# Kernel optimization log

Measured on AMD Instinct MI355X. Metric: run time of the kernel, lower is better.

Reference implementation:

```python
import jax, jax.numpy as jnp
import numpy as np

WS = 7       # window_size
SHIFT = 3    # shift_size
NH = 12      # num_heads
DIM = 384
EPS = 1e-5


def _rel_pos_index():
    coords = np.stack(np.meshgrid(np.arange(WS), np.arange(WS), indexing='ij'))  # [2,WS,WS]
    cf = coords.reshape(2, -1)
    rel = cf[:, :, None] - cf[:, None, :]              # [2,N,N]
    rel = rel.transpose(1, 2, 0)
    rel[:, :, 0] += WS - 1
    rel[:, :, 1] += WS - 1
    rel[:, :, 0] *= 2 * WS - 1
    return jnp.asarray(rel.sum(-1))                    # [N,N] int


def _attn_mask(H, W):
    img = np.zeros((H, W), dtype=np.float32)
    cnt = 0
    sl = (slice(0, -WS), slice(-WS, -SHIFT), slice(-SHIFT, None))
    for hs in sl:
        for ws in sl:
            img[hs, ws] = cnt
            cnt += 1
    mw = img.reshape(H // WS, WS, W // WS, WS).transpose(0, 2, 1, 3).reshape(-1, WS * WS)  # [nW,N]
    am = mw[:, None, :] - mw[:, :, None]
    am = np.where(am != 0, -100.0, 0.0).astype(np.float32)
    return jnp.asarray(am)                             # [nW,N,N]


def _ln(x, g, b):
    mu = jnp.mean(x, -1, keepdims=True)
    var = jnp.mean(jnp.square(x - mu), -1, keepdims=True)
    return (x - mu) * jax.lax.rsqrt(var + EPS) * g + b


def setup_inputs() -> dict:
    key = jax.random.key(0)
    ks = jax.random.split(key, 8)
    B, H, W, C = 32, 56, 56, DIM
    s = lambda fan: 1.0 / np.sqrt(fan)
    return {
        'x': jax.random.normal(ks[0], (B, H * W, C), jnp.float32),
        'ln1_g': jnp.ones((C,), jnp.float32), 'ln1_b': jnp.zeros((C,), jnp.float32),
        'qkv_w': jax.random.normal(ks[1], (C, 3 * C), jnp.float32) * s(C),
        'qkv_b': jnp.zeros((3 * C,), jnp.float32),
        'proj_w': jax.random.normal(ks[2], (C, C), jnp.float32) * s(C),
        'proj_b': jnp.zeros((C,), jnp.float32),
        'bias_table': jax.random.normal(ks[3], ((2 * WS - 1) ** 2, NH), jnp.float32) * 0.02,
        'ln2_g': jnp.ones((C,), jnp.float32), 'ln2_b': jnp.zeros((C,), jnp.float32),
        'fc1_w': jax.random.normal(ks[4], (C, 4 * C), jnp.float32) * s(C),
        'fc1_b': jnp.zeros((4 * C,), jnp.float32),
        'fc2_w': jax.random.normal(ks[5], (4 * C, C), jnp.float32) * s(4 * C),
        'fc2_b': jnp.zeros((C,), jnp.float32),
        'H': H, 'W': W,
    }


def reference(x, ln1_g, ln1_b, qkv_w, qkv_b, proj_w, proj_b, bias_table,
              ln2_g, ln2_b, fc1_w, fc1_b, fc2_w, fc2_b, H, W):
    B, L, C = x.shape
    N = WS * WS
    hd = C // NH
    scale = hd ** -0.5
    rel_idx = _rel_pos_index()
    mask = _attn_mask(H, W)          # [nW,N,N]
    nW = (H // WS) * (W // WS)

    shortcut = x
    h = _ln(x, ln1_g, ln1_b).reshape(B, H, W, C)
    h = jnp.roll(h, (-SHIFT, -SHIFT), axis=(1, 2))
    # window partition -> [B*nW, N, C]
    h = h.reshape(B, H // WS, WS, W // WS, WS, C).transpose(0, 1, 3, 2, 4, 5)
    h = h.reshape(B * nW, N, C)

    qkv = (h @ qkv_w + qkv_b).reshape(B * nW, N, 3, NH, hd).transpose(2, 0, 3, 1, 4)
    q, k, v = qkv[0] * scale, qkv[1], qkv[2]           # [B_,NH,N,hd]
    attn = jnp.einsum('bhnd,bhmd->bhnm', q, k)          # [B_,NH,N,N]
    rpb = bias_table[rel_idx].transpose(2, 0, 1)        # [NH,N,N]
    attn = attn + rpb[None]
    attn = attn.reshape(B, nW, NH, N, N) + mask[None, :, None]
    attn = jax.nn.softmax(attn.reshape(B * nW, NH, N, N), axis=-1)
    o = jnp.einsum('bhnm,bhmd->bhnd', attn, v).transpose(0, 2, 1, 3).reshape(B * nW, N, C)
    o = o @ proj_w + proj_b

    # window reverse + unshift
    o = o.reshape(B, H // WS, W // WS, WS, WS, C).transpose(0, 1, 3, 2, 4, 5).reshape(B, H, W, C)
    o = jnp.roll(o, (SHIFT, SHIFT), axis=(1, 2)).reshape(B, L, C)

    x = shortcut + o
    m = _ln(x, ln2_g, ln2_b)
    m = jax.nn.gelu(m @ fc1_w + fc1_b, approximate=False) @ fc2_w + fc2_b
    return x + m
```

## Files before the change

kernel.cpp:

```cpp
#include <hip/hip_runtime.h>
#include <hip/hip_bf16.h>
#include <math.h>

typedef __hip_bfloat16 bf16;
typedef __attribute__((ext_vector_type(8))) __bf16 bf16x8;
typedef __attribute__((ext_vector_type(4))) float f32x4;

#define SHIFT 3
#define TOK_TOTAL 100352
#define WIN_TOTAL 2048
#define BM_ELEMS (4 * 12 * 49 * 52)
#define PSTR 72

__device__ __forceinline__ bool is_f32(const void* flagp) {
  return ((const unsigned*)flagp)[0] == 0x3F800000u;
}
__device__ __forceinline__ float ldf(const void* p, size_t i, bool f32) {
  return f32 ? ((const float*)p)[i]
             : __bfloat162float(((const bf16*)p)[i]);
}

__global__ void cvt_small(const void* s0, const void* s1, const void* s2,
                          const void* s3, const void* s4, const void* s5,
                          const void* s6, const void* s7, const void* s8,
                          bf16* __restrict__ dst) {
  const bool f32 = is_f32(s0);
  int idx = blockIdx.x * 256 + threadIdx.x;
  if (idx >= 7020) return;
  const void* src; int off;
  if      (idx < 384)  { src = s0; off = 0; }
  else if (idx < 768)  { src = s1; off = 384; }
  else if (idx < 1920) { src = s2; off = 768; }
  else if (idx < 2304) { src = s3; off = 1920; }
  else if (idx < 4332) { src = s4; off = 2304; }
  else if (idx < 4716) { src = s5; off = 4332; }
  else if (idx < 5100) { src = s6; off = 4716; }
  else if (idx < 6636) { src = s7; off = 5100; }
  else                 { src = s8; off = 6636; }
  dst[idx] = __float2bfloat16(ldf(src, idx - off, f32));
}

__global__ void build_bm(const bf16* __restrict__ btab, bf16* __restrict__ bm) {
  int idx = blockIdx.x * 256 + threadIdx.x;
  if (idx >= 4 * 12 * 2401) return;
  int ch = idx / 2401, rem = idx - ch * 2401;
  int cls = ch / 12, head = ch - cls * 12;
  int q = rem / 49, k = rem - q * 49;
  int i1 = q / 7, j1 = q - 7 * i1;
  int i2 = k / 7, j2 = k - 7 * i2;
  int rel = (i1 - i2 + 6) * 13 + (j1 - j2 + 6);
  float v = __bfloat162float(btab[rel * 12 + head]);
  int rh1 = (cls & 2) ? (i1 < 4 ? 1 : 2) : 0;
  int rw1 = (cls & 1) ? (j1 < 4 ? 1 : 2) : 0;
  int rh2 = (cls & 2) ? (i2 < 4 ? 1 : 2) : 0;
  int rw2 = (cls & 1) ? (j2 < 4 ? 1 : 2) : 0;
  if (rh1 * 3 + rw1 != rh2 * 3 + rw2) v -= 100.0f;
  bm[(ch * 49 + q) * 52 + k] = __float2bfloat16(v);
}

__global__ void wt_transpose(const void* __restrict__ in, bf16* __restrict__ out,
                             int K, int N, const void* flagp) {
  const bool f32 = is_f32(flagp);
  int idx = blockIdx.x * 256 + threadIdx.x;
  if (idx < K * N) {
    int k = idx / N, n = idx - k * N;
    out[(size_t)n * K + k] = __float2bfloat16(ldf(in, idx, f32));
  }
}

__global__ __launch_bounds__(256) void ln1_impl(
    const void* __restrict__ x, const bf16* __restrict__ g,
    const bf16* __restrict__ b, bf16* __restrict__ h, int tokoff,
    const void* flagp) {
  const bool f32 = is_f32(flagp);
  int local = blockIdx.x * 4 + (threadIdx.x >> 6);
  int token = tokoff + local;
  int lane = threadIdx.x & 63;
  int w = token / 49, n = token - w * 49;
  int bb = w >> 6, iw = w & 63;
  int wh = iw >> 3, ww = iw & 7;
  int i = n / 7, j = n - i * 7;
  int sr = wh * 7 + i + SHIFT; if (sr >= 56) sr -= 56;
  int sc = ww * 7 + j + SHIFT; if (sc >= 56) sc -= 56;
  size_t base = ((size_t)bb * 3136 + (size_t)sr * 56 + sc) * 384;
  float v[6];
  float sum = 0.f, sq = 0.f;
#pragma unroll
  for (int t = 0; t < 6; t++) {
    v[t] = ldf(x, base + t * 64 + lane, f32);
    sum += v[t]; sq += v[t] * v[t];
  }
#pragma unroll
  for (int off = 32; off > 0; off >>= 1) {
    sum += __shfl_xor(sum, off);
    sq  += __shfl_xor(sq, off);
  }
  float mean = sum * (1.f / 384.f);
  float var  = sq * (1.f / 384.f) - mean * mean;
  float rstd = rsqrtf(var + 1e-5f);
  bf16* hp = h + (size_t)local * 384;
#pragma unroll
  for (int t = 0; t < 6; t++) {
    int c = t * 64 + lane;
    float y = (v[t] - mean) * rstd * __bfloat162float(g[c]) + __bfloat162float(b[c]);
    hp[c] = __float2bfloat16(y);
  }
}

__global__ __launch_bounds__(256) void ln2_kernel(
    const bf16* __restrict__ x1, const bf16* __restrict__ g,
    const bf16* __restrict__ b, bf16* __restrict__ out) {
  int local = blockIdx.x * 4 + (threadIdx.x >> 6);
  int lane = threadIdx.x & 63;
  const bf16* xp = x1 + (size_t)local * 384;
  float v[6];
  float sum = 0.f, sq = 0.f;
#pragma unroll
  for (int t = 0; t < 6; t++) {
    v[t] = __bfloat162float(xp[t * 64 + lane]);
    sum += v[t]; sq += v[t] * v[t];
  }
#pragma unroll
  for (int off = 32; off > 0; off >>= 1) {
    sum += __shfl_xor(sum, off);
    sq  += __shfl_xor(sq, off);
  }
  float mean = sum * (1.f / 384.f);
  float var  = sq * (1.f / 384.f) - mean * mean;
  float rstd = rsqrtf(var + 1e-5f);
  bf16* op = out + (size_t)local * 384;
#pragma unroll
  for (int t = 0; t < 6; t++) {
    int c = t * 64 + lane;
    float y = (v[t] - mean) * rstd * __bfloat162float(g[c]) + __bfloat162float(b[c]);
    op[c] = __float2bfloat16(y);
  }
}

template <int MODE>
__global__ __launch_bounds__(256, 2) void gemm128(
    const bf16* __restrict__ A, const bf16* __restrict__ Wt,
    const bf16* __restrict__ bias, void* __restrict__ outp,
    const void* __restrict__ extra, int K, int N, int tokoff,
    const void* flagp, int lbmask) {
  __shared__ bf16 As[128 * 40];
  __shared__ bf16 Bs[128 * 40];
  const int tid = threadIdx.x;
  const int wave = tid >> 6, lane = tid & 63;
  const int wm = (wave >> 1) * 64, wn = (wave & 1) * 64;
  const int lrow = lane & 15, lquad = lane >> 4;
  const int m0 = blockIdx.x * 128, n0 = blockIdx.y * 128;

  f32x4 acc[4][4] = {};

  const int arow = tid >> 2;
  const int acol = (tid & 3) * 8;
  const bf16* Ag = A + (size_t)(m0 + arow) * K + acol;
  const bf16* Bg = Wt + (size_t)(n0 + arow) * K + acol;
  const int ldso = arow * 40 + acol;

  for (int k0 = 0; k0 < K; k0 += 32) {
    float4 av0 = *(const float4*)(Ag + k0);
    float4 av1 = *(const float4*)(Ag + (size_t)64 * K + k0);
    float4 bv0 = *(const float4*)(Bg + k0);
    float4 bv1 = *(const float4*)(Bg + (size_t)64 * K + k0);
    __syncthreads();
    *(float4*)(As + ldso) = av0;
    *(float4*)(As + ldso + 64 * 40) = av1;
    *(float4*)(Bs + ldso) = bv0;
    *(float4*)(Bs + ldso + 64 * 40) = bv1;
    __syncthreads();
    bf16x8 af[4], bfr[4];
#pragma unroll
    for (int mi = 0; mi < 4; mi++)
      af[mi] = *(const bf16x8*)(As + (wm + mi * 16 + lrow) * 40 + lquad * 8);
#pragma unroll
    for (int ni = 0; ni < 4; ni++)
      bfr[ni] = *(const bf16x8*)(Bs + (wn + ni * 16 + lrow) * 40 + lquad * 8);
#pragma unroll
    for (int mi = 0; mi < 4; mi++)
#pragma unroll
      for (int ni = 0; ni < 4; ni++)
        acc[mi][ni] = __builtin_amdgcn_mfma_f32_16x16x32_bf16(
            af[mi], bfr[ni], acc[mi][ni], 0, 0, 0);
  }

  float bv[4];
#pragma unroll
  for (int ni = 0; ni < 4; ni++)
    bv[ni] = __bfloat162float(bias[n0 + wn + ni * 16 + lrow]);

  const bool f32 = (MODE == 1 || MODE == 3) ? is_f32(flagp) : false;

#pragma unroll
  for (int mi = 0; mi < 4; mi++) {
#pragma unroll
    for (int r = 0; r < 4; r++) {
      int row = m0 + wm + mi * 16 + lquad * 4 + r;
      if constexpr (MODE == 1) {
        bf16* xo = (bf16*)outp;
        int gtok = tokoff + row;
        int w = gtok / 49, n = gtok - w * 49;
        int bb = w >> 6, iw = w & 63;
        int wh = iw >> 3, ww = iw & 7;
        int i = n / 7, j = n - i * 7;
        int rr = wh * 7 + i + SHIFT; if (rr >= 56) rr -= 56;
        int cc = ww * 7 + j + SHIFT; if (cc >= 56) cc -= 56;
        int lb = bb & lbmask;
        size_t dloc = ((size_t)lb * 3136 + (size_t)rr * 56 + cc) * 384;
        size_t dglb = ((size_t)bb * 3136 + (size_t)rr * 56 + cc) * 384;
#pragma unroll
        for (int ni = 0; ni < 4; ni++) {
          int col = n0 + wn + ni * 16 + lrow;
          float v = acc[mi][ni][r] + bv[ni] + ldf(extra, dglb + col, f32);
          xo[dloc + col] = __float2bfloat16(v);
        }
      } else if constexpr (MODE == 3) {
        const bf16* x1 = (const bf16*)extra;
#pragma unroll
        for (int ni = 0; ni < 4; ni++) {
          int col = n0 + wn + ni * 16 + lrow;
          float v = acc[mi][ni][r] + bv[ni] + __bfloat162float(x1[(size_t)row * 384 + col]);
          size_t gi = (size_t)(tokoff + row) * 384 + col;
          if (f32) ((float*)outp)[gi] = v;
          else     ((bf16*)outp)[gi] = __float2bfloat16(v);
        }
      } else {
        bf16* xo = (bf16*)outp;
#pragma unroll
        for (int ni = 0; ni < 4; ni++) {
          int col = n0 + wn + ni * 16 + lrow;
          float v = acc[mi][ni][r] + bv[ni];
          if constexpr (MODE == 2)
            v = 0.5f * v * (1.0f + erff(v * 0.70710678118654752f));
          xo[(size_t)row * N + col] = __float2bfloat16(v);
        }
      }
    }
  }
}

__global__ __launch_bounds__(256) void attn_mfma(
    const bf16* __restrict__ qkv, const bf16* __restrict__ bm,
    bf16* __restrict__ out) {
  __shared__ bf16 pbuf[4][16 * PSTR];
  const int tid = threadIdx.x;
  const int wave = tid >> 6, lane = tid & 63;
  const int g = lane >> 4, lr = lane & 15;
  const int pair = blockIdx.x * 4 + wave;
  const int lw = pair / 12, head = pair - lw * 12;
  const int iw = lw & 63;
  const int wh = iw >> 3, ww = iw & 7;
  const int cls = ((wh == 7) ? 2 : 0) + ((ww == 7) ? 1 : 0);
  const bf16* bmh = bm + (size_t)(cls * 12 + head) * 49 * 52;
  const size_t qbase = (size_t)lw * 49 * 1152 + head * 32;
  bf16* pb = pbuf[wave];

  bf16x8 kf[4];
#pragma unroll
  for (int kj = 0; kj < 4; kj++) {
    int row = 16 * kj + lr; if (row > 48) row = 48;
    kf[kj] = *(const bf16x8*)(qkv + qbase + 384 + (size_t)row * 1152 + g * 8);
  }
  bf16x8 vf[2][2];
#pragma unroll
  for (int ks = 0; ks < 2; ks++)
#pragma unroll
    for (int di = 0; di < 2; di++) {
      union { bf16x8 v; short s[8]; } u;
#pragma unroll
      for (int j = 0; j < 8; j++) {
        int k = 32 * ks + 8 * g + j; if (k > 48) k = 48;
        u.s[j] = *(const short*)(qkv + qbase + 768 + (size_t)k * 1152 + 16 * di + lr);
      }
      vf[ks][di] = u.v;
    }

#pragma unroll
  for (int qi = 0; qi < 4; qi++) {
    int qrow = 16 * qi + lr; if (qrow > 48) qrow = 48;
    bf16x8 qf = *(const bf16x8*)(qkv + qbase + (size_t)qrow * 1152 + g * 8);
    f32x4 s[4] = {};
#pragma unroll
    for (int kj = 0; kj < 4; kj++)
      s[kj] = __builtin_amdgcn_mfma_f32_16x16x32_bf16(qf, kf[kj], s[kj], 0, 0, 0);

    float bmv[4][4];
#pragma unroll
    for (int r = 0; r < 4; r++) {
      int q = 16 * qi + 4 * g + r; if (q > 48) q = 48;
      const bf16* bmrow = bmh + q * 52;
#pragma unroll
      for (int kj = 0; kj < 4; kj++)
        bmv[r][kj] = __bfloat162float(bmrow[16 * kj + lr]);
    }

    float pexp[4][4];
    float inv[4];
#pragma unroll
    for (int r = 0; r < 4; r++) {
      float a[4];
#pragma unroll
      for (int kj = 0; kj < 4; kj++) {
        int k = 16 * kj + lr;
        a[kj] = (k < 49) ? fmaf(s[kj][r], 0.17677669529663687f, bmv[r][kj])
                         : -1e30f;
      }
      float m = fmaxf(fmaxf(a[0], a[1]), fmaxf(a[2], a[3]));
#pragma unroll
      for (int off = 8; off > 0; off >>= 1) m = fmaxf(m, __shfl_xor(m, off));
      float sum = 0.f;
#pragma unroll
      for (int kj = 0; kj < 4; kj++) {
        float e = __expf(a[kj] - m);
        pexp[kj][r] = e; sum += e;
      }
#pragma unroll
      for (int off = 8; off > 0; off >>= 1) sum += __shfl_xor(sum, off);
      inv[r] = 1.0f / sum;
    }

#pragma unroll
    for (int kj = 0; kj < 4; kj++)
#pragma unroll
      for (int r = 0; r < 4; r++)
        pb[(4 * g + r) * PSTR + 16 * kj + lr] = __float2bfloat16(pexp[kj][r]);

    bf16x8 pf0 = *(const bf16x8*)(pb + lr * PSTR + g * 8);
    bf16x8 pf1 = *(const bf16x8*)(pb + lr * PSTR + 32 + g * 8);

    f32x4 o[2] = {};
    o[0] = __builtin_amdgcn_mfma_f32_16x16x32_bf16(pf0, vf[0][0], o[0], 0, 0, 0);
    o[0] = __builtin_amdgcn_mfma_f32_16x16x32_bf16(pf1, vf[1][0], o[0], 0, 0, 0);
    o[1] = __builtin_amdgcn_mfma_f32_16x16x32_bf16(pf0, vf[0][1], o[1], 0, 0, 0);
    o[1] = __builtin_amdgcn_mfma_f32_16x16x32_bf16(pf1, vf[1][1], o[1], 0, 0, 0);

#pragma unroll
    for (int r = 0; r < 4; r++) {
      int q = 16 * qi + 4 * g + r;
      if (q < 49) {
#pragma unroll
        for (int di = 0; di < 2; di++)
          out[(size_t)(lw * 49 + q) * 384 + head * 32 + 16 * di + lr] =
              __float2bfloat16(o[di][r] * inv[r]);
      }
    }
  }
}

extern "C" void kernel_launch(void* const* d_in, const int* in_sizes, int n_in,
                              void* d_out, int out_size, void* d_ws, size_t ws_size,
                              hipStream_t stream) {
  const void* x          = d_in[0];
  const void* ln1_g      = d_in[1];
  const void* ln1_b      = d_in[2];
  const void* qkv_w      = d_in[3];
  const void* qkv_b      = d_in[4];
  const void* proj_w     = d_in[5];
  const void* proj_b     = d_in[6];
  const void* bias_table = d_in[7];
  const void* ln2_g      = d_in[8];
  const void* ln2_b      = d_in[9];
  const void* fc1_w      = d_in[10];
  const void* fc1_b      = d_in[11];
  const void* fc2_w      = d_in[12];
  const void* fc2_b      = d_in[13];

  char* ws = (char*)d_ws;
  bf16* qkv_wt  = (bf16*)ws;
  bf16* proj_wt = qkv_wt + 1152 * 384;
  bf16* fc1_wt  = proj_wt + 384 * 384;
  bf16* fc2_wt  = fc1_wt + 1536 * 384;
  bf16* small   = fc2_wt + 384 * 1536;
  bf16* bmtab   = small + 8192;
  char* p = (char*)(bmtab + BM_ELEMS + 64);

  const size_t fixedB = (size_t)(p - ws);
  int nchunk = 16;
  for (int n = 1; n <= 16; n <<= 1) {
    size_t need = fixedB + (size_t)(TOK_TOTAL / n) * 4608;
    if (need <= ws_size) { nchunk = n; break; }
  }
  const int CH   = TOK_TOTAL / nchunk;
  const int CWIN = WIN_TOTAL / nchunk;
  const int lbmask = 32 / nchunk - 1;

  bf16* buf1   = (bf16*)p;
  bf16* buf_x1 = (bf16*)(p + (size_t)CH * 384 * 2);
  bf16* buf2   = (bf16*)(p + (size_t)CH * 384 * 4);

  const bf16* c_ln1g = small;
  const bf16* c_ln1b = small + 384;
  const bf16* c_qkvb = small + 768;
  const bf16* c_projb = small + 1920;
  const bf16* c_btab = small + 2304;
  const bf16* c_ln2g = small + 4332;
  const bf16* c_ln2b = small + 4716;
  const bf16* c_fc1b = small + 5100;
  const bf16* c_fc2b = small + 6636;

  cvt_small<<<dim3(28), 256, 0, stream>>>(ln1_g, ln1_b, qkv_b, proj_b, bias_table,
                                          ln2_g, ln2_b, fc1_b, fc2_b, small);
  build_bm<<<dim3((4 * 12 * 2401 + 255) / 256), 256, 0, stream>>>(c_btab, bmtab);

  wt_transpose<<<dim3((384 * 1152 + 255) / 256), 256, 0, stream>>>(qkv_w, qkv_wt, 384, 1152, ln1_g);
  wt_transpose<<<dim3((384 * 384  + 255) / 256), 256, 0, stream>>>(proj_w, proj_wt, 384, 384, ln1_g);
  wt_transpose<<<dim3((384 * 1536 + 255) / 256), 256, 0, stream>>>(fc1_w, fc1_wt, 384, 1536, ln1_g);
  wt_transpose<<<dim3((1536 * 384 + 255) / 256), 256, 0, stream>>>(fc2_w, fc2_wt, 1536, 384, ln1_g);

  for (int c = 0; c < nchunk; c++) {
    const int tokoff = c * CH;

    ln1_impl<<<dim3(CH / 4), 256, 0, stream>>>(x, c_ln1g, c_ln1b, buf1, tokoff, ln1_g);

    gemm128<0><<<dim3(CH / 128, 9), 256, 0, stream>>>(
        buf1, qkv_wt, c_qkvb, buf2, nullptr, 384, 1152, 0, ln1_g, 0);

    attn_mfma<<<dim3(CWIN * 12 / 4), 256, 0, stream>>>(buf2, bmtab, buf1);

    gemm128<1><<<dim3(CH / 128, 3), 256, 0, stream>>>(
        buf1, proj_wt, c_projb, buf_x1, x, 384, 384, tokoff, ln1_g, lbmask);

    ln2_kernel<<<dim3(CH / 4), 256, 0, stream>>>(buf_x1, c_ln2g, c_ln2b, buf1);

    gemm128<2><<<dim3(CH / 128, 12), 256, 0, stream>>>(
        buf1, fc1_wt, c_fc1b, buf2, nullptr, 384, 1536, 0, ln1_g, 0);

    gemm128<3><<<dim3(CH / 128, 3), 256, 0, stream>>>(
        buf2, fc2_wt, c_fc2b, d_out, buf_x1, 1536, 384, tokoff, ln1_g, 0);
  }
}
```

Before: 1.258 ms.

## Fuse MLP fc1+GELU+fc2 into one kernel and swap GEMM grid axes

Replaces the separate fc1 (with GELU) and fc2 GEMM launches with one fused kernel. Each block handles 64 tokens, computes 128-wide slices of the hidden activation into LDS, applies GELU, and accumulates the fc2 product directly. This removes the large hidden-activation round trip through global memory and cuts the workspace need, which may allow fewer chunks. Separately, the remaining GEMMs now use the N tiles as the fast grid axis so neighbouring blocks share A rows. The cost is that fc2 weights are read straight from global memory with no LDS staging, and the 64-token tile gives less reuse per block.

```diff
diff --git a/kernel.cpp b/kernel.cpp
--- a/kernel.cpp
+++ b/kernel.cpp
@@ -149,7 +149,7 @@
   const int wave = tid >> 6, lane = tid & 63;
   const int wm = (wave >> 1) * 64, wn = (wave & 1) * 64;
   const int lrow = lane & 15, lquad = lane >> 4;
-  const int m0 = blockIdx.x * 128, n0 = blockIdx.y * 128;
+  const int m0 = blockIdx.y * 128, n0 = blockIdx.x * 128;
 
   f32x4 acc[4][4] = {};
 
@@ -190,7 +190,7 @@
   for (int ni = 0; ni < 4; ni++)
     bv[ni] = __bfloat162float(bias[n0 + wn + ni * 16 + lrow]);
 
-  const bool f32 = (MODE == 1 || MODE == 3) ? is_f32(flagp) : false;
+  const bool f32 = (MODE == 1) ? is_f32(flagp) : false;
 
 #pragma unroll
   for (int mi = 0; mi < 4; mi++) {
@@ -215,29 +215,122 @@
           float v = acc[mi][ni][r] + bv[ni] + ldf(extra, dglb + col, f32);
           xo[dloc + col] = __float2bfloat16(v);
         }
-      } else if constexpr (MODE == 3) {
-        const bf16* x1 = (const bf16*)extra;
-#pragma unroll
-        for (int ni = 0; ni < 4; ni++) {
-          int col = n0 + wn + ni * 16 + lrow;
-          float v = acc[mi][ni][r] + bv[ni] + __bfloat162float(x1[(size_t)row * 384 + col]);
-          size_t gi = (size_t)(tokoff + row) * 384 + col;
-          if (f32) ((float*)outp)[gi] = v;
-          else     ((bf16*)outp)[gi] = __float2bfloat16(v);
-        }
       } else {
         bf16* xo = (bf16*)outp;
 #pragma unroll
         for (int ni = 0; ni < 4; ni++) {
           int col = n0 + wn + ni * 16 + lrow;
           float v = acc[mi][ni][r] + bv[ni];
-          if constexpr (MODE == 2)
-            v = 0.5f * v * (1.0f + erff(v * 0.70710678118654752f));
           xo[(size_t)row * N + col] = __float2bfloat16(v);
         }
       }
     }
   }
+}
+
+__global__ __launch_bounds__(256, 2) void mlp_fused(
+    const bf16* __restrict__ A,
+    const bf16* __restrict__ W1t,
+    const bf16* __restrict__ W2t,
+    const bf16* __restrict__ b1,
+    const bf16* __restrict__ b2,
+    const bf16* __restrict__ x1,
+    void* __restrict__ outp, int tokoff, const void* flagp) {
+  __shared__ bf16 As[64 * 40];
+  __shared__ bf16 Bs[128 * 40];
+  __shared__ bf16 Pl[64 * 136];
+  const int tid = threadIdx.x;
+  const int wave = tid >> 6, lane = tid & 63;
+  const int lr = lane & 15, g = lane >> 4;
+  const int tok0 = blockIdx.x * 64;
+
+  f32x4 acc2[4][6] = {};
+
+  const int srow = tid >> 2, scol = (tid & 3) * 8;
+  const bf16* Ag = A + (size_t)(tok0 + srow) * 384 + scol;
+  const int ldso = srow * 40 + scol;
+
+  for (int kk = 0; kk < 12; kk++) {
+    f32x4 pacc[4][2] = {};
+    const bf16* Bg = W1t + (size_t)(kk * 128 + srow) * 384 + scol;
+    for (int k0 = 0; k0 < 384; k0 += 32) {
+      float4 av  = *(const float4*)(Ag + k0);
+      float4 bv0 = *(const float4*)(Bg + k0);
+      float4 bv1 = *(const float4*)(Bg + (size_t)64 * 384 + k0);
+      __syncthreads();
+      *(float4*)(As + ldso) = av;
+      *(float4*)(Bs + ldso) = bv0;
+      *(float4*)(Bs + ldso + 64 * 40) = bv1;
+      __syncthreads();
+      bf16x8 af[4], bw[2];
+#pragma unroll
+      for (int mi = 0; mi < 4; mi++)
+        af[mi] = *(const bf16x8*)(As + (mi * 16 + lr) * 40 + g * 8);
+#pragma unroll
+      for (int ni = 0; ni < 2; ni++)
+        bw[ni] = *(const bf16x8*)(Bs + (wave * 32 + ni * 16 + lr) * 40 + g * 8);
+#pragma unroll
+      for (int mi = 0; mi < 4; mi++)
+#pragma unroll
+        for (int ni = 0; ni < 2; ni++)
+          pacc[mi][ni] = __builtin_amdgcn_mfma_f32_16x16x32_bf16(
+              af[mi], bw[ni], pacc[mi][ni], 0, 0, 0);
+    }
+    float b1v[2];
+#pragma unroll
+    for (int ni = 0; ni < 2; ni++)
+      b1v[ni] = __bfloat162float(b1[kk * 128 + wave * 32 + ni * 16 + lr]);
+#pragma unroll
+    for (int mi = 0; mi < 4; mi++)
+#pragma unroll
+      for (int ni = 0; ni < 2; ni++)
+#pragma unroll
+        for (int r = 0; r < 4; r++) {
+          float v = pacc[mi][ni][r] + b1v[ni];
+          v = 0.5f * v * (1.0f + erff(v * 0.70710678118654752f));
+          Pl[(mi * 16 + g * 4 + r) * 136 + wave * 32 + ni * 16 + lr] =
+              __float2bfloat16(v);
+        }
+    __syncthreads();
+    const int kb = kk * 128;
+#pragma unroll
+    for (int kk2 = 0; kk2 < 4; kk2++) {
+      bf16x8 pf[4];
+#pragma unroll
+      for (int mi = 0; mi < 4; mi++)
+        pf[mi] = *(const bf16x8*)(Pl + (mi * 16 + lr) * 136 + kk2 * 32 + g * 8);
+#pragma unroll
+      for (int ni = 0; ni < 6; ni++) {
+        bf16x8 wf = *(const bf16x8*)(
+            W2t + (size_t)(wave * 96 + ni * 16 + lr) * 1536 + kb + kk2 * 32 + g * 8);
+#pragma unroll
+        for (int mi = 0; mi < 4; mi++)
+          acc2[mi][ni] = __builtin_amdgcn_mfma_f32_16x16x32_bf16(
+              pf[mi], wf, acc2[mi][ni], 0, 0, 0);
+      }
+    }
+  }
+
+  const bool f32o = is_f32(flagp);
+  float b2v[6];
+#pragma unroll
+  for (int ni = 0; ni < 6; ni++)
+    b2v[ni] = __bfloat162float(b2[wave * 96 + ni * 16 + lr]);
+#pragma unroll
+  for (int mi = 0; mi < 4; mi++)
+#pragma unroll
+    for (int r = 0; r < 4; r++) {
+      int row = mi * 16 + g * 4 + r;
+      size_t lt = (size_t)(tok0 + row) * 384;
+      size_t gt = (size_t)(tokoff + tok0 + row) * 384;
+#pragma unroll
+      for (int ni = 0; ni < 6; ni++) {
+        int col = wave * 96 + ni * 16 + lr;
+        float v = acc2[mi][ni][r] + b2v[ni] + __bfloat162float(x1[lt + col]);
+        if (f32o) ((float*)outp)[gt + col] = v;
+        else      ((bf16*)outp)[gt + col] = __float2bfloat16(v);
+      }
+    }
 }
 
 __global__ __launch_bounds__(256) void attn_mfma(
@@ -378,7 +471,7 @@
   const size_t fixedB = (size_t)(p - ws);
   int nchunk = 16;
   for (int n = 1; n <= 16; n <<= 1) {
-    size_t need = fixedB + (size_t)(TOK_TOTAL / n) * 4608;
+    size_t need = fixedB + (size_t)(TOK_TOTAL / n) * 3840;
     if (need <= ws_size) { nchunk = n; break; }
   }
   const int CH   = TOK_TOTAL / nchunk;
@@ -413,20 +506,17 @@
 
     ln1_impl<<<dim3(CH / 4), 256, 0, stream>>>(x, c_ln1g, c_ln1b, buf1, tokoff, ln1_g);
 
-    gemm128<0><<<dim3(CH / 128, 9), 256, 0, stream>>>(
+    gemm128<0><<<dim3(9, CH / 128), 256, 0, stream>>>(
         buf1, qkv_wt, c_qkvb, buf2, nullptr, 384, 1152, 0, ln1_g, 0);
 
     attn_mfma<<<dim3(CWIN * 12 / 4), 256, 0, stream>>>(buf2, bmtab, buf1);
 
-    gemm128<1><<<dim3(CH / 128, 3), 256, 0, stream>>>(
+    gemm128<1><<<dim3(3, CH / 128), 256, 0, stream>>>(
         buf1, proj_wt, c_projb, buf_x1, x, 384, 384, tokoff, ln1_g, lbmask);
 
     ln2_kernel<<<dim3(CH / 4), 256, 0, stream>>>(buf_x1, c_ln2g, c_ln2b, buf1);
 
-    gemm128<2><<<dim3(CH / 128, 12), 256, 0, stream>>>(
-        buf1, fc1_wt, c_fc1b, buf2, nullptr, 384, 1536, 0, ln1_g, 0);
-
-    gemm128<3><<<dim3(CH / 128, 3), 256, 0, stream>>>(
-        buf2, fc2_wt, c_fc2b, d_out, buf_x1, 1536, 384, tokoff, ln1_g, 0);
-  }
-}
+    mlp_fused<<<dim3(CH / 64), 256, 0, stream>>>(
+        buf1, fc1_wt, fc2_wt, c_fc1b, c_fc2b, buf_x1, d_out, tokoff, ln1_g);
+  }
+}
```

After: 1.463 ms. +16.3%, slower.

## Double-buffer GEMM tiles via direct global-to-LDS loads with swizzle

Applied to the files above, without the earlier changes.

The GEMM main loop now uses global_load_lds to copy A/B tiles straight into a double-buffered, XOR-swizzled LDS layout, prefetching the next k-slice while MFMAs run on the current one. Launch bounds rise to 4 blocks per CU, and the grid is reordered so N tiles vary fastest, which lets weight tiles be shared across neighbouring blocks. The chunk count now starts at 4 instead of 1. The aim is to remove the register round trip and the exposed load latency between syncs, at the cost of register pressure at the higher occupancy and a correctness risk in the swizzle and async-load ordering.

```diff
diff --git a/kernel.cpp b/kernel.cpp
--- a/kernel.cpp
+++ b/kernel.cpp
@@ -18,6 +18,12 @@
 __device__ __forceinline__ float ldf(const void* p, size_t i, bool f32) {
   return f32 ? ((const float*)p)[i]
              : __bfloat162float(((const bf16*)p)[i]);
+}
+
+__device__ __forceinline__ void gload16(const bf16* g, bf16* l) {
+  __builtin_amdgcn_global_load_lds(
+      (const __attribute__((address_space(1))) unsigned int*)g,
+      (__attribute__((address_space(3))) unsigned int*)l, 16, 0, 0);
 }
 
 __global__ void cvt_small(const void* s0, const void* s1, const void* s2,
@@ -138,51 +144,63 @@
 }
 
 template <int MODE>
-__global__ __launch_bounds__(256, 2) void gemm128(
+__global__ __launch_bounds__(256, 4) void gemm128(
     const bf16* __restrict__ A, const bf16* __restrict__ Wt,
     const bf16* __restrict__ bias, void* __restrict__ outp,
     const void* __restrict__ extra, int K, int N, int tokoff,
     const void* flagp, int lbmask) {
-  __shared__ bf16 As[128 * 40];
-  __shared__ bf16 Bs[128 * 40];
+  __shared__ bf16 As[2][128 * 32];
+  __shared__ bf16 Bs[2][128 * 32];
   const int tid = threadIdx.x;
   const int wave = tid >> 6, lane = tid & 63;
   const int wm = (wave >> 1) * 64, wn = (wave & 1) * 64;
   const int lrow = lane & 15, lquad = lane >> 4;
-  const int m0 = blockIdx.x * 128, n0 = blockIdx.y * 128;
+  const int m0 = blockIdx.y * 128, n0 = blockIdx.x * 128;
 
   f32x4 acc[4][4] = {};
 
-  const int arow = tid >> 2;
-  const int acol = (tid & 3) * 8;
-  const bf16* Ag = A + (size_t)(m0 + arow) * K + acol;
-  const bf16* Bg = Wt + (size_t)(n0 + arow) * K + acol;
-  const int ldso = arow * 40 + acol;
-
-  for (int k0 = 0; k0 < K; k0 += 32) {
-    float4 av0 = *(const float4*)(Ag + k0);
-    float4 av1 = *(const float4*)(Ag + (size_t)64 * K + k0);
-    float4 bv0 = *(const float4*)(Bg + k0);
-    float4 bv1 = *(const float4*)(Bg + (size_t)64 * K + k0);
-    __syncthreads();
-    *(float4*)(As + ldso) = av0;
-    *(float4*)(As + ldso + 64 * 40) = av1;
-    *(float4*)(Bs + ldso) = bv0;
-    *(float4*)(Bs + ldso + 64 * 40) = bv1;
-    __syncthreads();
+  const int srow = lane >> 2;
+  const int sst  = (srow ^ (srow >> 2)) & 3;
+  const int scol = (((lane & 3) ^ sst) * 8);
+  const int slab0 = wave * 2;
+  const bf16* Ar0 = A  + (size_t)(m0 + slab0 * 16 + srow) * K + scol;
+  const bf16* Ar1 = A  + (size_t)(m0 + slab0 * 16 + 16 + srow) * K + scol;
+  const bf16* Br0 = Wt + (size_t)(n0 + slab0 * 16 + srow) * K + scol;
+  const bf16* Br1 = Wt + (size_t)(n0 + slab0 * 16 + 16 + srow) * K + scol;
+
+  const int rsw = ((lrow ^ (lrow >> 2)) & 3) * 8;
+  const int rchunk = (lquad * 8) ^ rsw;
+
+  const int nk = K >> 5;
+  gload16(Ar0, &As[0][slab0 * 512]);
+  gload16(Ar1, &As[0][slab0 * 512 + 512]);
+  gload16(Br0, &Bs[0][slab0 * 512]);
+  gload16(Br1, &Bs[0][slab0 * 512 + 512]);
+  __syncthreads();
+
+  for (int t = 0; t < nk; t++) {
+    const int cur = t & 1;
+    if (t + 1 < nk) {
+      const int k0 = (t + 1) << 5;
+      gload16(Ar0 + k0, &As[cur ^ 1][slab0 * 512]);
+      gload16(Ar1 + k0, &As[cur ^ 1][slab0 * 512 + 512]);
+      gload16(Br0 + k0, &Bs[cur ^ 1][slab0 * 512]);
+      gload16(Br1 + k0, &Bs[cur ^ 1][slab0 * 512 + 512]);
+    }
     bf16x8 af[4], bfr[4];
 #pragma unroll
     for (int mi = 0; mi < 4; mi++)
-      af[mi] = *(const bf16x8*)(As + (wm + mi * 16 + lrow) * 40 + lquad * 8);
+      af[mi] = *(const bf16x8*)&As[cur][(wm + mi * 16 + lrow) * 32 + rchunk];
 #pragma unroll
     for (int ni = 0; ni < 4; ni++)
-      bfr[ni] = *(const bf16x8*)(Bs + (wn + ni * 16 + lrow) * 40 + lquad * 8);
+      bfr[ni] = *(const bf16x8*)&Bs[cur][(wn + ni * 16 + lrow) * 32 + rchunk];
 #pragma unroll
     for (int mi = 0; mi < 4; mi++)
 #pragma unroll
       for (int ni = 0; ni < 4; ni++)
         acc[mi][ni] = __builtin_amdgcn_mfma_f32_16x16x32_bf16(
             af[mi], bfr[ni], acc[mi][ni], 0, 0, 0);
+    __syncthreads();
   }
 
   float bv[4];
@@ -377,7 +395,7 @@
 
   const size_t fixedB = (size_t)(p - ws);
   int nchunk = 16;
-  for (int n = 1; n <= 16; n <<= 1) {
+  for (int n = 4; n <= 16; n <<= 1) {
     size_t need = fixedB + (size_t)(TOK_TOTAL / n) * 4608;
     if (need <= ws_size) { nchunk = n; break; }
   }
@@ -413,20 +431,20 @@
 
     ln1_impl<<<dim3(CH / 4), 256, 0, stream>>>(x, c_ln1g, c_ln1b, buf1, tokoff, ln1_g);
 
-    gemm128<0><<<dim3(CH / 128, 9), 256, 0, stream>>>(
+    gemm128<0><<<dim3(9, CH / 128), 256, 0, stream>>>(
         buf1, qkv_wt, c_qkvb, buf2, nullptr, 384, 1152, 0, ln1_g, 0);
 
     attn_mfma<<<dim3(CWIN * 12 / 4), 256, 0, stream>>>(buf2, bmtab, buf1);
 
-    gemm128<1><<<dim3(CH / 128, 3), 256, 0, stream>>>(
+    gemm128<1><<<dim3(3, CH / 128), 256, 0, stream>>>(
         buf1, proj_wt, c_projb, buf_x1, x, 384, 384, tokoff, ln1_g, lbmask);
 
     ln2_kernel<<<dim3(CH / 4), 256, 0, stream>>>(buf_x1, c_ln2g, c_ln2b, buf1);
 
-    gemm128<2><<<dim3(CH / 128, 12), 256, 0, stream>>>(
+    gemm128<2><<<dim3(12, CH / 128), 256, 0, stream>>>(
         buf1, fc1_wt, c_fc1b, buf2, nullptr, 384, 1536, 0, ln1_g, 0);
 
-    gemm128<3><<<dim3(CH / 128, 3), 256, 0, stream>>>(
+    gemm128<3><<<dim3(3, CH / 128), 256, 0, stream>>>(
         buf2, fc2_wt, c_fc2b, d_out, buf_x1, 1536, 384, tokoff, ln1_g, 0);
   }
 }
```

Measured after the change: 1.284 ms. +2.1%, slower.

## Load GEMM fragments directly from global memory with register double-buffering

Applied to the files above, without the earlier changes.

The GEMM kernel no longer stages tiles through LDS. Each wave loads its MFMA operand fragments straight from global memory into registers, double-buffered across two K-steps, which removes the __syncthreads barriers and LDS traffic. Grid axes are swapped so consecutive blocks share the same A rows (N tiles vary fastest), and launch bounds rise to 3 blocks per CU. The trade-off is that A and B fragments are re-read from global/L2 by each wave instead of being shared through LDS, and the extra register buffers add register pressure.

```diff
diff --git a/kernel.cpp b/kernel.cpp
--- a/kernel.cpp
+++ b/kernel.cpp
@@ -138,52 +138,57 @@
 }
 
 template <int MODE>
-__global__ __launch_bounds__(256, 2) void gemm128(
+__global__ __launch_bounds__(256, 3) void gemm128(
     const bf16* __restrict__ A, const bf16* __restrict__ Wt,
     const bf16* __restrict__ bias, void* __restrict__ outp,
     const void* __restrict__ extra, int K, int N, int tokoff,
     const void* flagp, int lbmask) {
-  __shared__ bf16 As[128 * 40];
-  __shared__ bf16 Bs[128 * 40];
   const int tid = threadIdx.x;
   const int wave = tid >> 6, lane = tid & 63;
   const int wm = (wave >> 1) * 64, wn = (wave & 1) * 64;
   const int lrow = lane & 15, lquad = lane >> 4;
-  const int m0 = blockIdx.x * 128, n0 = blockIdx.y * 128;
+  const int m0 = blockIdx.y * 128, n0 = blockIdx.x * 128;
 
   f32x4 acc[4][4] = {};
 
-  const int arow = tid >> 2;
-  const int acol = (tid & 3) * 8;
-  const bf16* Ag = A + (size_t)(m0 + arow) * K + acol;
-  const bf16* Bg = Wt + (size_t)(n0 + arow) * K + acol;
-  const int ldso = arow * 40 + acol;
-
-  for (int k0 = 0; k0 < K; k0 += 32) {
-    float4 av0 = *(const float4*)(Ag + k0);
-    float4 av1 = *(const float4*)(Ag + (size_t)64 * K + k0);
-    float4 bv0 = *(const float4*)(Bg + k0);
-    float4 bv1 = *(const float4*)(Bg + (size_t)64 * K + k0);
-    __syncthreads();
-    *(float4*)(As + ldso) = av0;
-    *(float4*)(As + ldso + 64 * 40) = av1;
-    *(float4*)(Bs + ldso) = bv0;
-    *(float4*)(Bs + ldso + 64 * 40) = bv1;
-    __syncthreads();
-    bf16x8 af[4], bfr[4];
-#pragma unroll
-    for (int mi = 0; mi < 4; mi++)
-      af[mi] = *(const bf16x8*)(As + (wm + mi * 16 + lrow) * 40 + lquad * 8);
-#pragma unroll
-    for (int ni = 0; ni < 4; ni++)
-      bfr[ni] = *(const bf16x8*)(Bs + (wn + ni * 16 + lrow) * 40 + lquad * 8);
-#pragma unroll
-    for (int mi = 0; mi < 4; mi++)
-#pragma unroll
-      for (int ni = 0; ni < 4; ni++)
-        acc[mi][ni] = __builtin_amdgcn_mfma_f32_16x16x32_bf16(
-            af[mi], bfr[ni], acc[mi][ni], 0, 0, 0);
-  }
+  const bf16* Ap = A  + (size_t)(m0 + wm + lrow) * K + lquad * 8;
+  const bf16* Bp = Wt + (size_t)(n0 + wn + lrow) * K + lquad * 8;
+  const size_t rowK16 = (size_t)16 * K;
+
+  bf16x8 a0_0, a0_1, a0_2, a0_3, b0_0, b0_1, b0_2, b0_3;
+  bf16x8 a1_0, a1_1, a1_2, a1_3, b1_0, b1_1, b1_2, b1_3;
+
+#define LOADSET(sfx, kk)                                         \
+  a##sfx##_0 = *(const bf16x8*)(Ap + 0 * rowK16 + (kk));         \
+  a##sfx##_1 = *(const bf16x8*)(Ap + 1 * rowK16 + (kk));         \
+  a##sfx##_2 = *(const bf16x8*)(Ap + 2 * rowK16 + (kk));         \
+  a##sfx##_3 = *(const bf16x8*)(Ap + 3 * rowK16 + (kk));         \
+  b##sfx##_0 = *(const bf16x8*)(Bp + 0 * rowK16 + (kk));         \
+  b##sfx##_1 = *(const bf16x8*)(Bp + 1 * rowK16 + (kk));         \
+  b##sfx##_2 = *(const bf16x8*)(Bp + 2 * rowK16 + (kk));         \
+  b##sfx##_3 = *(const bf16x8*)(Bp + 3 * rowK16 + (kk));
+
+#define MFMASET(sfx)                                                          \
+  {                                                                           \
+    const bf16x8 af_[4] = {a##sfx##_0, a##sfx##_1, a##sfx##_2, a##sfx##_3};   \
+    const bf16x8 bf_[4] = {b##sfx##_0, b##sfx##_1, b##sfx##_2, b##sfx##_3};   \
+    _Pragma("unroll")                                                         \
+    for (int mi = 0; mi < 4; mi++)                                            \
+      _Pragma("unroll")                                                       \
+      for (int ni = 0; ni < 4; ni++)                                          \
+        acc[mi][ni] = __builtin_amdgcn_mfma_f32_16x16x32_bf16(                \
+            af_[mi], bf_[ni], acc[mi][ni], 0, 0, 0);                          \
+  }
+
+  LOADSET(0, 0);
+  for (int k0 = 0; k0 < K; k0 += 64) {
+    LOADSET(1, k0 + 32);
+    MFMASET(0);
+    if (k0 + 64 < K) { LOADSET(0, k0 + 64); }
+    MFMASET(1);
+  }
+#undef LOADSET
+#undef MFMASET
 
   float bv[4];
 #pragma unroll
@@ -413,20 +418,20 @@
 
     ln1_impl<<<dim3(CH / 4), 256, 0, stream>>>(x, c_ln1g, c_ln1b, buf1, tokoff, ln1_g);
 
-    gemm128<0><<<dim3(CH / 128, 9), 256, 0, stream>>>(
+    gemm128<0><<<dim3(9, CH / 128), 256, 0, stream>>>(
         buf1, qkv_wt, c_qkvb, buf2, nullptr, 384, 1152, 0, ln1_g, 0);
 
     attn_mfma<<<dim3(CWIN * 12 / 4), 256, 0, stream>>>(buf2, bmtab, buf1);
 
-    gemm128<1><<<dim3(CH / 128, 3), 256, 0, stream>>>(
+    gemm128<1><<<dim3(3, CH / 128), 256, 0, stream>>>(
         buf1, proj_wt, c_projb, buf_x1, x, 384, 384, tokoff, ln1_g, lbmask);
 
     ln2_kernel<<<dim3(CH / 4), 256, 0, stream>>>(buf_x1, c_ln2g, c_ln2b, buf1);
 
-    gemm128<2><<<dim3(CH / 128, 12), 256, 0, stream>>>(
+    gemm128<2><<<dim3(12, CH / 128), 256, 0, stream>>>(
         buf1, fc1_wt, c_fc1b, buf2, nullptr, 384, 1536, 0, ln1_g, 0);
 
-    gemm128<3><<<dim3(CH / 128, 3), 256, 0, stream>>>(
+    gemm128<3><<<dim3(3, CH / 128), 256, 0, stream>>>(
         buf2, fc2_wt, c_fc2b, d_out, buf_x1, 1536, 384, tokoff, ln1_g, 0);
   }
 }
```

After: 1.896 ms. 1.51x slower.
